# Kernel tuning notes

Hardware: AMD Instinct MI355X
Metric: run time of the kernel (lower is better)

Reference implementation:

```python
import jax, jax.numpy as jnp
import numpy as np

BS, D, S, K = 32, 64, 2048, 1024  # batch, embedding_dim, seq_len, num_embeddings


def setup_inputs() -> dict:
    key = jax.random.key(0)
    k1, k2 = jax.random.split(key)
    x = jax.random.normal(k1, (BS, D, S), dtype=jnp.float32)
    # xavier_uniform on [D, K]
    bound = float(np.sqrt(6.0 / (D + K)))
    embeddings = jax.random.uniform(k2, (D, K), dtype=jnp.float32, minval=-bound, maxval=bound)
    return {"x": x, "embeddings": embeddings}


def reference(x, embeddings):
    bs, d, s = x.shape
    k = embeddings.shape[1]
    # [bs, d, s] -> [bs*s, d]
    flat = x.transpose(0, 2, 1).reshape(-1, d)
    unquantized = flat
    # squared distance ||a||^2 - 2 a.b + ||b||^2 -> [N, K]
    a2 = jnp.sum(flat * flat, axis=1, keepdims=True)
    ab2 = 2.0 * (flat @ embeddings)
    b2 = jnp.sum(embeddings * embeddings, axis=0, keepdims=True)
    distance = a2 - ab2 + b2
    encoding_indices = jnp.argmin(distance, axis=1)  # == (-distance).argmax(1)
    one_hot = jax.nn.one_hot(encoding_indices, k, dtype=jnp.int32)  # F.one_hot -> int
    quantized = jnp.take(embeddings.T, encoding_indices, axis=0)  # [N, d] gather
    quantized = quantized.reshape(bs, s, d).transpose(0, 2, 1)  # [bs, d, s]
    e_latent_loss = jnp.mean(jnp.square(quantized - jax.lax.stop_gradient(x)))
    q_latent_loss = jnp.mean(jnp.square(jax.lax.stop_gradient(quantized) - x))
    loss = q_latent_loss + e_latent_loss
    # straight-through estimator
    quantized_st = x + jax.lax.stop_gradient(quantized - x)
    return (
        quantized_st,
        loss,
        one_hot.reshape(bs, s, k).transpose(0, 2, 1),
        encoding_indices.reshape(bs, s),
        distance.reshape(bs, s, k).transpose(0, 2, 1),
        unquantized,
        embeddings.T,
    )
```

## Files before the change

### kernel.cpp

```cpp
#include <hip/hip_runtime.h>

#define BSZ 32
#define DIM 64
#define SEQ 2048
#define KE  1024
#define KC  128
#define ST  128

#define O0 0ull
#define O1 4194304ull
#define O2 4194305ull
#define O3 71303169ull
#define O4 71368705ull
#define O5 138477569ull
#define O6 142671873ull

struct __attribute__((packed, aligned(4))) F4 { float x, y, z, w; };

__device__ __forceinline__ void lds_barrier() {
    asm volatile("s_waitcnt lgkmcnt(0)" ::: "memory");
    __builtin_amdgcn_s_barrier();
}

__global__ __launch_bounds__(256) void vq_prep(const float* __restrict__ E,
                                               float* __restrict__ out,
                                               float* __restrict__ et_ws,
                                               float* __restrict__ b2_ws) {
    __shared__ float T[64][65];
    const int tid  = threadIdx.x;
    const int lane = tid & 63;
    const int sub  = tid >> 6;
    const int k0   = blockIdx.x * 64;
    for (int dd = 0; dd < 16; ++dd) {
        int d = dd * 4 + sub;
        T[d][lane] = E[(size_t)d * KE + k0 + lane];
    }
    __syncthreads();
    for (int ii = 0; ii < 16; ++ii) {
        int kl = ii * 4 + sub;
        float v = T[lane][kl];
        out[O6 + (size_t)(k0 + kl) * 64 + lane] = v;
        et_ws[(size_t)(k0 + kl) * 64 + lane]    = v;
    }
    if (tid < 64) {
        float s = 0.f;
        #pragma unroll
        for (int d = 0; d < 64; ++d) {
            float v = T[d][tid];
            s = fmaf(v, v, s);
        }
        b2_ws[k0 + tid] = s;
    }
    if (blockIdx.x == 0 && tid == 0) out[O1] = 0.f;
}

__global__ __launch_bounds__(256, 2) void vq_main(const float* __restrict__ x,
                                                  const float* __restrict__ E,
                                                  const float* __restrict__ et,
                                                  const float* __restrict__ b2,
                                                  float* __restrict__ out) {
    __shared__ __align__(16) float xt[64 * ST];
    __shared__ __align__(16) union UU {
        float e[64 * KC];
        struct { float D[16][ST]; int Kk[16][ST]; } red;
        float qt[64 * ST];
    } u;
    __shared__ __align__(16) float a2s[ST];

    const int tid = threadIdx.x;
    const int tx  = tid & 15;
    const int ky  = tid >> 4;
    const int b   = blockIdx.x >> 4;
    const int s0  = (blockIdx.x & 15) << 7;
    const int sq  = tx << 2;

    float4 er[8];
    #pragma unroll
    for (int i = 0; i < 8; ++i) {
        int f = (i << 8) + tid, d = f >> 5, j = f & 31;
        er[i] = *(const float4*)(E + (size_t)d * KE + (j << 2));
    }
    {
        const float* xb = x + ((size_t)b << 17) + s0;
        #pragma unroll
        for (int i = 0; i < 8; ++i) {
            int f = (i << 8) + tid, d = f >> 5, j = f & 31;
            *(float4*)&xt[d * ST + (j << 2)] =
                *(const float4*)(xb + ((size_t)d << 11) + (j << 2));
        }
    }
    __syncthreads();
    if (tid < ST) {
        float sacc = 0.f;
        #pragma unroll
        for (int d = 0; d < 64; ++d) { float v = xt[d * ST + tid]; sacc = fmaf(v, v, sacc); }
        a2s[tid] = sacc;
    }

    float bD[8]; int bK[8];
    #pragma unroll
    for (int j = 0; j < 8; ++j) { bD[j] = 3.4e38f; bK[j] = 0; }

    float* outD = out + O4 + ((size_t)b << 21) + s0;
    float* outH = out + O2 + ((size_t)b << 21) + s0;

    #pragma unroll 1
    for (int c = 0; c < KE / KC; ++c) {
        const int kc = c << 7;
        lds_barrier();
        #pragma unroll
        for (int i = 0; i < 8; ++i) {
            int f = (i << 8) + tid, d = f >> 5, j = f & 31;
            *(float4*)&u.e[d * KC + (j << 2)] = er[i];
        }
        lds_barrier();
        if (c < KE / KC - 1) {
            #pragma unroll
            for (int i = 0; i < 8; ++i) {
                int f = (i << 8) + tid, d = f >> 5, j = f & 31;
                er[i] = *(const float4*)(E + (size_t)d * KE + (kc + KC) + (j << 2));
            }
        }

        float acc[8][8];
        #pragma unroll
        for (int jk = 0; jk < 8; ++jk)
            #pragma unroll
            for (int js = 0; js < 8; ++js) acc[jk][js] = 0.f;

        #pragma unroll 2
        for (int d = 0; d < 64; ++d) {
            const float* xp = &xt[d * ST + sq];
            const float* ep = &u.e[d * KC + (ky << 3)];
            float4 xa = *(const float4*)xp;
            float4 xb4 = *(const float4*)(xp + 64);
            float4 ea = *(const float4*)ep;
            float4 eb4 = *(const float4*)(ep + 4);
            float xs[8] = {xa.x, xa.y, xa.z, xa.w, xb4.x, xb4.y, xb4.z, xb4.w};
            float es[8] = {ea.x, ea.y, ea.z, ea.w, eb4.x, eb4.y, eb4.z, eb4.w};
            #pragma unroll
            for (int jk = 0; jk < 8; ++jk)
                #pragma unroll
                for (int js = 0; js < 8; ++js)
                    acc[jk][js] = fmaf(es[jk], xs[js], acc[jk][js]);
        }

        float4 b2a = *(const float4*)(b2 + kc + (ky << 3));
        float4 b2b = *(const float4*)(b2 + kc + (ky << 3) + 4);
        float b2v[8] = {b2a.x, b2a.y, b2a.z, b2a.w, b2b.x, b2b.y, b2b.z, b2b.w};
        float4 av1 = *(const float4*)&a2s[sq];
        float4 av2 = *(const float4*)&a2s[sq + 64];
        float a2v[8] = {av1.x, av1.y, av1.z, av1.w, av2.x, av2.y, av2.z, av2.w};
        #pragma unroll
        for (int jk = 0; jk < 8; ++jk) {
            const int k = kc + (ky << 3) + jk;
            float dv[8];
            #pragma unroll
            for (int js = 0; js < 8; ++js) {
                dv[js] = fmaf(-2.f, acc[jk][js], a2v[js] + b2v[jk]);
                if (dv[js] < bD[js]) { bD[js] = dv[js]; bK[js] = k; }
            }
            float* pD = outD + ((size_t)k << 11);
            float* pH = outH + ((size_t)k << 11);
            *(F4*)(pD + sq)      = F4{dv[0], dv[1], dv[2], dv[3]};
            *(F4*)(pD + 64 + sq) = F4{dv[4], dv[5], dv[6], dv[7]};
            *(F4*)(pH + sq)      = F4{0.f, 0.f, 0.f, 0.f};
            *(F4*)(pH + 64 + sq) = F4{0.f, 0.f, 0.f, 0.f};
        }
    }

    lds_barrier();
    #pragma unroll
    for (int js = 0; js < 8; ++js) {
        int sl = sq + (js & 3) + ((js >> 2) << 6);
        u.red.D[ky][sl]  = bD[js];
        u.red.Kk[ky][sl] = bK[js];
    }
    __syncthreads();

    if (tid < ST) {
        float bDr = u.red.D[0][tid];
        int   bKr = u.red.Kk[0][tid];
        #pragma unroll
        for (int w = 1; w < 16; ++w) {
            float dw = u.red.D[w][tid];
            int   kw = u.red.Kk[w][tid];
            if (dw < bDr || (dw == bDr && kw < bKr)) { bDr = dw; bKr = kw; }
        }
        out[O3 + (size_t)b * SEQ + s0 + tid] = (float)bKr;
        out[O2 + ((size_t)b << 21) + ((size_t)bKr << 11) + s0 + tid] = 1.f;

        const float* q = et + ((size_t)bKr << 6);
        float lsum = 0.f;
        #pragma unroll
        for (int i = 0; i < 16; ++i) {
            float4 q4 = ((const float4*)q)[i];
            float qs[4] = {q4.x, q4.y, q4.z, q4.w};
            #pragma unroll
            for (int j = 0; j < 4; ++j) {
                int d = i * 4 + j;
                u.qt[d * ST + tid] = qs[j];
                float df = qs[j] - xt[d * ST + tid];
                lsum = fmaf(df, df, lsum);
            }
        }
        #pragma unroll
        for (int m = 32; m >= 1; m >>= 1) lsum += __shfl_xor(lsum, m, 64);
        if ((tid & 63) == 0) atomicAdd(out + O1, lsum * (2.f / 4194304.f));
    }
    __syncthreads();

    {
        float* oq = out + ((size_t)b << 17) + s0;
        #pragma unroll
        for (int i = 0; i < 8; ++i) {
            int f = (i << 8) + tid, d = f >> 5, sc = (f & 31) << 2;
            *(float4*)(oq + ((size_t)d << 11) + sc) = *(const float4*)&u.qt[d * ST + sc];
        }
    }
    {
        const int lane = tid & 63, sub = tid >> 6;
        float* op = out + O5 + (((size_t)b << 11) + s0) * 64;
        #pragma unroll
        for (int ii = 0; ii < 16; ++ii) {
            int sl = ii * 4 + sub;
            op[(size_t)sl * 64 + lane] = xt[lane * ST + sl];
        }
    }
}

extern "C" void kernel_launch(void* const* d_in, const int* in_sizes, int n_in,
                              void* d_out, int out_size, void* d_ws, size_t ws_size,
                              hipStream_t stream) {
    const float* x = (const float*)d_in[0];
    const float* E = (const float*)d_in[1];
    float* out   = (float*)d_out;
    float* et_ws = (float*)d_ws;
    float* b2_ws = et_ws + 65536;
    vq_prep<<<16, 256, 0, stream>>>(E, out, et_ws, b2_ws);
    vq_main<<<512, 256, 0, stream>>>(x, E, et_ws, b2_ws, out);
}
```

Before: 247.4 us.

## Double threads per block and write quantized output directly from registers

The main kernel now runs 512 threads per block. Each thread computes an 8x4 tile of distances instead of 8x8, which halves accumulator registers and spreads the large distance and one-hot stores over more waves. The LDS staging buffer for the quantized output is removed: the reduction threads write quantized values straight to global memory, dropping one barrier and a copy pass. The launch bound of 512 threads with 4 blocks may force a tight VGPR cap and cause spills. Each thread now issues fewer FMAs per LDS load, so the inner loop does less compute per load.

```diff
diff --git a/kernel.cpp b/kernel.cpp
--- a/kernel.cpp
+++ b/kernel.cpp
@@ -54,7 +54,7 @@
     if (blockIdx.x == 0 && tid == 0) out[O1] = 0.f;
 }
 
-__global__ __launch_bounds__(256, 2) void vq_main(const float* __restrict__ x,
+__global__ __launch_bounds__(512, 4) void vq_main(const float* __restrict__ x,
                                                   const float* __restrict__ E,
                                                   const float* __restrict__ et,
                                                   const float* __restrict__ b2,
@@ -63,28 +63,27 @@
     __shared__ __align__(16) union UU {
         float e[64 * KC];
         struct { float D[16][ST]; int Kk[16][ST]; } red;
-        float qt[64 * ST];
     } u;
     __shared__ __align__(16) float a2s[ST];
 
     const int tid = threadIdx.x;
-    const int tx  = tid & 15;
-    const int ky  = tid >> 4;
+    const int tx  = tid & 31;
+    const int ky  = tid >> 5;
     const int b   = blockIdx.x >> 4;
     const int s0  = (blockIdx.x & 15) << 7;
     const int sq  = tx << 2;
 
-    float4 er[8];
+    float4 er[4];
     #pragma unroll
-    for (int i = 0; i < 8; ++i) {
-        int f = (i << 8) + tid, d = f >> 5, j = f & 31;
+    for (int i = 0; i < 4; ++i) {
+        int f = (i << 9) + tid, d = f >> 5, j = f & 31;
         er[i] = *(const float4*)(E + (size_t)d * KE + (j << 2));
     }
     {
         const float* xb = x + ((size_t)b << 17) + s0;
         #pragma unroll
-        for (int i = 0; i < 8; ++i) {
-            int f = (i << 8) + tid, d = f >> 5, j = f & 31;
+        for (int i = 0; i < 4; ++i) {
+            int f = (i << 9) + tid, d = f >> 5, j = f & 31;
             *(float4*)&xt[d * ST + (j << 2)] =
                 *(const float4*)(xb + ((size_t)d << 11) + (j << 2));
         }
@@ -97,9 +96,9 @@
         a2s[tid] = sacc;
     }
 
-    float bD[8]; int bK[8];
+    float bD[4]; int bK[4];
     #pragma unroll
-    for (int j = 0; j < 8; ++j) { bD[j] = 3.4e38f; bK[j] = 0; }
+    for (int j = 0; j < 4; ++j) { bD[j] = 3.4e38f; bK[j] = 0; }
 
     float* outD = out + O4 + ((size_t)b << 21) + s0;
     float* outH = out + O2 + ((size_t)b << 21) + s0;
@@ -109,72 +108,65 @@
         const int kc = c << 7;
         lds_barrier();
         #pragma unroll
-        for (int i = 0; i < 8; ++i) {
-            int f = (i << 8) + tid, d = f >> 5, j = f & 31;
+        for (int i = 0; i < 4; ++i) {
+            int f = (i << 9) + tid, d = f >> 5, j = f & 31;
             *(float4*)&u.e[d * KC + (j << 2)] = er[i];
         }
         lds_barrier();
         if (c < KE / KC - 1) {
             #pragma unroll
-            for (int i = 0; i < 8; ++i) {
-                int f = (i << 8) + tid, d = f >> 5, j = f & 31;
+            for (int i = 0; i < 4; ++i) {
+                int f = (i << 9) + tid, d = f >> 5, j = f & 31;
                 er[i] = *(const float4*)(E + (size_t)d * KE + (kc + KC) + (j << 2));
             }
         }
 
-        float acc[8][8];
+        float acc[8][4];
         #pragma unroll
         for (int jk = 0; jk < 8; ++jk)
             #pragma unroll
-            for (int js = 0; js < 8; ++js) acc[jk][js] = 0.f;
+            for (int js = 0; js < 4; ++js) acc[jk][js] = 0.f;
 
         #pragma unroll 2
         for (int d = 0; d < 64; ++d) {
-            const float* xp = &xt[d * ST + sq];
-            const float* ep = &u.e[d * KC + (ky << 3)];
-            float4 xa = *(const float4*)xp;
-            float4 xb4 = *(const float4*)(xp + 64);
-            float4 ea = *(const float4*)ep;
-            float4 eb4 = *(const float4*)(ep + 4);
-            float xs[8] = {xa.x, xa.y, xa.z, xa.w, xb4.x, xb4.y, xb4.z, xb4.w};
-            float es[8] = {ea.x, ea.y, ea.z, ea.w, eb4.x, eb4.y, eb4.z, eb4.w};
+            float4 xa = *(const float4*)&xt[d * ST + sq];
+            float4 ea = *(const float4*)&u.e[d * KC + (ky << 3)];
+            float4 eb = *(const float4*)&u.e[d * KC + (ky << 3) + 4];
+            float xs[4] = {xa.x, xa.y, xa.z, xa.w};
+            float es[8] = {ea.x, ea.y, ea.z, ea.w, eb.x, eb.y, eb.z, eb.w};
             #pragma unroll
             for (int jk = 0; jk < 8; ++jk)
                 #pragma unroll
-                for (int js = 0; js < 8; ++js)
+                for (int js = 0; js < 4; ++js)
                     acc[jk][js] = fmaf(es[jk], xs[js], acc[jk][js]);
         }
 
         float4 b2a = *(const float4*)(b2 + kc + (ky << 3));
         float4 b2b = *(const float4*)(b2 + kc + (ky << 3) + 4);
         float b2v[8] = {b2a.x, b2a.y, b2a.z, b2a.w, b2b.x, b2b.y, b2b.z, b2b.w};
-        float4 av1 = *(const float4*)&a2s[sq];
-        float4 av2 = *(const float4*)&a2s[sq + 64];
-        float a2v[8] = {av1.x, av1.y, av1.z, av1.w, av2.x, av2.y, av2.z, av2.w};
+        float4 av = *(const float4*)&a2s[sq];
+        float a2v[4] = {av.x, av.y, av.z, av.w};
         #pragma unroll
         for (int jk = 0; jk < 8; ++jk) {
             const int k = kc + (ky << 3) + jk;
-            float dv[8];
-            #pragma unroll
-            for (int js = 0; js < 8; ++js) {
+            float dv[4];
+            #pragma unroll
+            for (int js = 0; js < 4; ++js) {
                 dv[js] = fmaf(-2.f, acc[jk][js], a2v[js] + b2v[jk]);
                 if (dv[js] < bD[js]) { bD[js] = dv[js]; bK[js] = k; }
             }
             float* pD = outD + ((size_t)k << 11);
             float* pH = outH + ((size_t)k << 11);
-            *(F4*)(pD + sq)      = F4{dv[0], dv[1], dv[2], dv[3]};
-            *(F4*)(pD + 64 + sq) = F4{dv[4], dv[5], dv[6], dv[7]};
-            *(F4*)(pH + sq)      = F4{0.f, 0.f, 0.f, 0.f};
-            *(F4*)(pH + 64 + sq) = F4{0.f, 0.f, 0.f, 0.f};
+            *(F4*)(pD + sq) = F4{dv[0], dv[1], dv[2], dv[3]};
+            *(F4*)(pH + sq) = F4{0.f, 0.f, 0.f, 0.f};
         }
     }
 
     lds_barrier();
     #pragma unroll
-    for (int js = 0; js < 8; ++js) {
-        int sl = sq + (js & 3) + ((js >> 2) << 6);
-        u.red.D[ky][sl]  = bD[js];
-        u.red.Kk[ky][sl] = bK[js];
+    for (int js = 0; js < 4; ++js) {
+        u.red.D[ky][sq + js]  = bD[js];
+        u.red.Kk[ky][sq + js] = bK[js];
     }
     __syncthreads();
 
@@ -191,6 +183,7 @@
         out[O2 + ((size_t)b << 21) + ((size_t)bKr << 11) + s0 + tid] = 1.f;
 
         const float* q = et + ((size_t)bKr << 6);
+        float* outQ = out + ((size_t)b << 17) + s0 + tid;
         float lsum = 0.f;
         #pragma unroll
         for (int i = 0; i < 16; ++i) {
@@ -199,7 +192,7 @@
             #pragma unroll
             for (int j = 0; j < 4; ++j) {
                 int d = i * 4 + j;
-                u.qt[d * ST + tid] = qs[j];
+                outQ[(size_t)d << 11] = qs[j];
                 float df = qs[j] - xt[d * ST + tid];
                 lsum = fmaf(df, df, lsum);
             }
@@ -208,22 +201,13 @@
         for (int m = 32; m >= 1; m >>= 1) lsum += __shfl_xor(lsum, m, 64);
         if ((tid & 63) == 0) atomicAdd(out + O1, lsum * (2.f / 4194304.f));
     }
-    __syncthreads();
-
-    {
-        float* oq = out + ((size_t)b << 17) + s0;
-        #pragma unroll
-        for (int i = 0; i < 8; ++i) {
-            int f = (i << 8) + tid, d = f >> 5, sc = (f & 31) << 2;
-            *(float4*)(oq + ((size_t)d << 11) + sc) = *(const float4*)&u.qt[d * ST + sc];
-        }
-    }
+
     {
         const int lane = tid & 63, sub = tid >> 6;
         float* op = out + O5 + (((size_t)b << 11) + s0) * 64;
         #pragma unroll
         for (int ii = 0; ii < 16; ++ii) {
-            int sl = ii * 4 + sub;
+            int sl = ii * 8 + sub;
             op[(size_t)sl * 64 + lane] = xt[lane * ST + sl];
         }
     }
@@ -238,5 +222,5 @@
     float* et_ws = (float*)d_ws;
     float* b2_ws = et_ws + 65536;
     vq_prep<<<16, 256, 0, stream>>>(E, out, et_ws, b2_ws);
-    vq_main<<<512, 256, 0, stream>>>(x, E, et_ws, b2_ws, out);
-}
+    vq_main<<<512, 512, 0, stream>>>(x, E, et_ws, b2_ws, out);
+}
```

Result: faster. 238.8 us (-3.5%).
